# Performance work log

Measured on AMD Instinct MI355X. Metric: run time of the kernel, lower is better.

Reference implementation:

```python
import jax, jax.numpy as jnp
import numpy as np

B, N, DIM = 4, 2048, 1024
HEADS, DIM_HEAD = 16, 64
SCALE = DIM_HEAD ** -0.5


def setup_inputs() -> dict:
    key = jax.random.key(0)
    ks = jax.random.split(key, 5)
    x = jax.random.normal(ks[0], (B, N, DIM), dtype=jnp.float32)
    s = DIM ** -0.5
    Wq = jax.random.normal(ks[1], (DIM, HEADS * DIM_HEAD), dtype=jnp.float32) * s
    Wk = jax.random.normal(ks[2], (DIM, HEADS * DIM_HEAD), dtype=jnp.float32) * s
    Wv = jax.random.normal(ks[3], (DIM, HEADS * DIM_HEAD), dtype=jnp.float32) * s
    Wo = jax.random.normal(ks[4], (HEADS * DIM_HEAD, DIM), dtype=jnp.float32) * s
    bo = jnp.zeros((DIM,), dtype=jnp.float32)
    return {"x": x, "Wq": Wq, "Wk": Wk, "Wv": Wv, "Wo": Wo, "bo": bo}


def reference(x, Wq, Wk, Wv, Wo, bo):
    b, n, _ = x.shape
    # project and split heads: [b, n, h, d] -> [b, h, n, d]
    def split_heads(t):
        return t.reshape(b, n, HEADS, DIM_HEAD).transpose(0, 2, 1, 3)
    q = split_heads(x @ Wq)
    k = split_heads(x @ Wk)
    v = split_heads(x @ Wv)
    dots = jnp.einsum("bhid,bhjd->bhij", q, k) * SCALE  # [b,h,n,n]
    attn = jax.nn.softmax(dots, axis=-1)
    out = jnp.einsum("bhij,bhjd->bhid", attn, v)  # [b,h,n,d]
    out = out.transpose(0, 2, 1, 3).reshape(b, n, HEADS * DIM_HEAD)
    # project_out is True (heads != 1); dropout is identity at inference
    return out @ Wo + bo
```

## Files before the change

### kernel.cpp

```cpp
#include <hip/hip_runtime.h>
#include <stdint.h>

typedef __attribute__((ext_vector_type(8))) short short8;
typedef __attribute__((ext_vector_type(8))) unsigned short u16x8;
typedef __attribute__((ext_vector_type(4))) float f32x4;

#define DEV static __device__ __forceinline__

DEV unsigned short f2bf(float f) {
  unsigned u = __builtin_bit_cast(unsigned, f);
  u += 0x7FFF + ((u >> 16) & 1);
  return (unsigned short)(u >> 16);
}

DEV unsigned cvtpk_bf16(float lo, float hi) {
  unsigned r;
  asm("v_cvt_pk_bf16_f32 %0, %1, %2" : "=v"(r) : "v"(lo), "v"(hi));
  return r;
}

#define GLOAD16(gptr, lptr)                                                        \
  __builtin_amdgcn_global_load_lds((const __attribute__((address_space(1))) void*)(gptr), \
                                   (__attribute__((address_space(3))) void*)(lptr), 16, 0, 0)

__global__ __launch_bounds__(256) void k_cast_x(const float* __restrict__ in,
                                                unsigned short* __restrict__ out) {
  int idx = (blockIdx.x * 256 + threadIdx.x) * 8;
  float4 a = *(const float4*)(in + idx);
  float4 b = *(const float4*)(in + idx + 4);
  u16x8 v;
  v[0] = f2bf(a.x); v[1] = f2bf(a.y); v[2] = f2bf(a.z); v[3] = f2bf(a.w);
  v[4] = f2bf(b.x); v[5] = f2bf(b.y); v[6] = f2bf(b.z); v[7] = f2bf(b.w);
  *(u16x8*)(out + idx) = v;
}

__global__ __launch_bounds__(256) void k_transW(const float* __restrict__ wq,
                                                const float* __restrict__ wk,
                                                const float* __restrict__ wv,
                                                const float* __restrict__ wo,
                                                unsigned short* __restrict__ wqkvT,
                                                unsigned short* __restrict__ woT) {
  __shared__ __align__(16) unsigned short t[64 * 72];
  int z = blockIdx.z;
  const float* src = (z == 0) ? wq : (z == 1) ? wk : (z == 2) ? wv : wo;
  unsigned short* dst = (z < 3) ? (wqkvT + (size_t)z * 1048576) : woT;
  int r0 = blockIdx.y * 64;
  int c0 = blockIdx.x * 64;
  int tid = threadIdx.x;
#pragma unroll
  for (int it = 0; it < 4; ++it) {
    int idx = it * 256 + tid;
    int il = idx >> 4;
    int c4 = idx & 15;
    float4 v = *(const float4*)(src + (size_t)(r0 + il) * 1024 + c0 + c4 * 4);
    t[(c4 * 4 + 0) * 72 + il] = f2bf(v.x);
    t[(c4 * 4 + 1) * 72 + il] = f2bf(v.y);
    t[(c4 * 4 + 2) * 72 + il] = f2bf(v.z);
    t[(c4 * 4 + 3) * 72 + il] = f2bf(v.w);
  }
  __syncthreads();
#pragma unroll
  for (int it = 0; it < 2; ++it) {
    int idx = it * 256 + tid;
    int ol = idx >> 3;
    int ch = idx & 7;
    *(u16x8*)(dst + (size_t)(c0 + ol) * 1024 + r0 + ch * 8) =
        *(const u16x8*)(t + ol * 72 + ch * 8);
  }
}

template <int MODE>
__global__ __launch_bounds__(256) void k_gemm(const unsigned short* __restrict__ A,
                                              const unsigned short* __restrict__ Bt,
                                              unsigned short* __restrict__ outB,
                                              unsigned short* __restrict__ vTout,
                                              float* __restrict__ outF,
                                              const float* __restrict__ bias) {
  __shared__ __align__(16) unsigned short sA[128 * 64];
  __shared__ __align__(16) unsigned short sB[128 * 64];
  const int tid = threadIdx.x;
  const int l = tid & 63;
  const int w = tid >> 6;

  const int lid = blockIdx.x;
  const int nwg = (MODE == 0) ? 1536 : 512;
  const int swz = (lid & 7) * (nwg >> 3) + (lid >> 3);
  const int z = (MODE == 0) ? (swz >> 9) : 0;
  const int rem = (MODE == 0) ? (swz & 511) : swz;
  const int m0 = (rem >> 3) * 128;
  const int n0 = (rem & 7) * 128;

  const int wm = (w >> 1) * 64;
  const int wn = (w & 1) * 64;
  const int q16 = l & 15, g4 = l >> 4;
  const int lrow = l >> 3;
  const int lsw = ((l & 7) ^ lrow) * 8;

  const unsigned short* bt = Bt + (size_t)z * 1048576;
  unsigned short* dst = outB + (size_t)z * 8388608;
  const float sc = (MODE == 0 && z == 0) ? 0.125f * 1.44269504088896f : 1.0f;

  f32x4 acc[4][4];
#pragma unroll
  for (int i = 0; i < 4; ++i)
#pragma unroll
    for (int j = 0; j < 4; ++j) acc[i][j] = (f32x4){0.f, 0.f, 0.f, 0.f};

  for (int k0 = 0; k0 < 1024; k0 += 64) {
    __syncthreads();
#pragma unroll
    for (int r = 0; r < 4; ++r) {
      int chunk = w * 4 + r;
      int row = chunk * 8 + lrow;
      GLOAD16(A + (size_t)(m0 + row) * 1024 + k0 + lsw, sA + chunk * 512);
      GLOAD16(bt + (size_t)(n0 + row) * 1024 + k0 + lsw, sB + chunk * 512);
    }
    __syncthreads();
#pragma unroll
    for (int kk = 0; kk < 2; ++kk) {
      short8 af[4], bf_[4];
#pragma unroll
      for (int i = 0; i < 4; ++i) {
        int ra = wm + i * 16 + q16;
        af[i] = *(const short8*)(sA + ra * 64 + (((kk * 4 + g4) ^ (ra & 7)) * 8));
        int rb = wn + i * 16 + q16;
        bf_[i] = *(const short8*)(sB + rb * 64 + (((kk * 4 + g4) ^ (rb & 7)) * 8));
      }
#pragma unroll
      for (int mi = 0; mi < 4; ++mi)
#pragma unroll
        for (int ni = 0; ni < 4; ++ni)
          acc[mi][ni] =
              __builtin_amdgcn_mfma_f32_16x16x32_bf16(af[mi], bf_[ni], acc[mi][ni], 0, 0, 0);
    }
  }

  if (MODE == 0 && z == 2) {
#pragma unroll
    for (int mi = 0; mi < 4; ++mi) {
#pragma unroll
      for (int ni = 0; ni < 4; ++ni) {
        int row0 = m0 + wm + mi * 16 + g4 * 4;
        int col = n0 + wn + ni * 16 + q16;
        int b = row0 >> 11, seq0 = row0 & 2047;
        int h = col >> 6, d = col & 63;
        uint2 pv;
        pv.x = cvtpk_bf16(acc[mi][ni][0], acc[mi][ni][1]);
        pv.y = cvtpk_bf16(acc[mi][ni][2], acc[mi][ni][3]);
        *(uint2*)(vTout + (((size_t)(b * 16 + h) * 64 + d) * 2048 + seq0)) = pv;
      }
    }
  } else {
#pragma unroll
    for (int mi = 0; mi < 4; ++mi) {
#pragma unroll
      for (int ni = 0; ni < 4; ++ni) {
#pragma unroll
        for (int j = 0; j < 4; ++j) {
          int row = m0 + wm + mi * 16 + g4 * 4 + j;
          int col = n0 + wn + ni * 16 + q16;
          float val = acc[mi][ni][j];
          if (MODE == 0) {
            val *= sc;
            int b = row >> 11, seq = row & 2047;
            int h = col >> 6, d = col & 63;
            dst[((((size_t)b * 16 + h) * 2048 + seq) << 6) + d] = f2bf(val);
          } else {
            outF[(size_t)row * 1024 + col] = val + bias[col];
          }
        }
      }
    }
  }
}

__global__ __launch_bounds__(512) void k_attn(const unsigned short* __restrict__ Q,
                                              const unsigned short* __restrict__ Kg,
                                              const unsigned short* __restrict__ Vt,
                                              unsigned short* __restrict__ Oo) {
  __shared__ __align__(16) unsigned short sK[4][64 * 64];
  __shared__ __align__(16) unsigned short sV[4][64 * 64];
  __shared__ __align__(16) unsigned short sP[8][16 * 64];
  const int tid = threadIdx.x;
  const int l = tid & 63, w = tid >> 6;
  const int q16 = l & 15, g = l >> 4;
  const int bh = blockIdx.y;
  const int q0 = blockIdx.x * 128 + w * 16;
  const int lrow = l >> 3;
  const int lsw = ((l & 7) ^ lrow) * 8;

  const unsigned short* Qb = Q + ((size_t)bh * 2048 + q0) * 64;
  const unsigned short* Kb = Kg + (size_t)bh * 2048 * 64;
  const unsigned short* Vb = Vt + (size_t)bh * 64 * 2048;

  short8 qf[2];
#pragma unroll
  for (int s = 0; s < 2; ++s) qf[s] = *(const short8*)(Qb + q16 * 64 + s * 32 + g * 8);

  float sum = 0.f;
  f32x4 o[4];
#pragma unroll
  for (int dt = 0; dt < 4; ++dt) o[dt] = (f32x4){0.f, 0.f, 0.f, 0.f};

  auto STAGE = [&](int slot, int kv) {
    int row = w * 8 + lrow;
    GLOAD16(Kb + (size_t)(kv + row) * 64 + lsw, &sK[slot][w * 512]);
    GLOAD16(Vb + (size_t)row * 2048 + kv + lsw, &sV[slot][w * 512]);
  };

  auto COMPUTE = [&](int slot) {
    f32x4 st[4];
    __builtin_amdgcn_s_setprio(1);
#pragma unroll
    for (int t = 0; t < 4; ++t) {
      st[t] = (f32x4){0.f, 0.f, 0.f, 0.f};
#pragma unroll
      for (int s = 0; s < 2; ++s) {
        int key = t * 16 + q16;
        short8 kf = *(const short8*)(&sK[slot][key * 64 + (((s * 4 + g) ^ (key & 7)) * 8)]);
        st[t] = __builtin_amdgcn_mfma_f32_16x16x32_bf16(kf, qf[s], st[t], 0, 0, 0);
      }
    }
    __builtin_amdgcn_s_setprio(0);

    float p[4][4];
    float ps = 0.f;
#pragma unroll
    for (int t = 0; t < 4; ++t)
#pragma unroll
      for (int j = 0; j < 4; ++j) {
        p[t][j] = __builtin_amdgcn_exp2f(st[t][j]);
        ps += p[t][j];
      }
    ps += __shfl_xor(ps, 16);
    ps += __shfl_xor(ps, 32);
    sum += ps;

#pragma unroll
    for (int t = 0; t < 4; ++t) {
      uint2 pv;
      pv.x = cvtpk_bf16(p[t][0], p[t][1]);
      pv.y = cvtpk_bf16(p[t][2], p[t][3]);
      int c16 = t * 2 + (g >> 1);
      *(uint2*)(&sP[w][q16 * 64 + ((c16 ^ (q16 & 7)) * 8) + (g & 1) * 4]) = pv;
    }
    asm volatile("s_waitcnt lgkmcnt(0)" ::: "memory");
    __builtin_amdgcn_sched_barrier(0);

    __builtin_amdgcn_s_setprio(1);
#pragma unroll
    for (int win = 0; win < 2; ++win) {
      short8 pf = *(const short8*)(&sP[w][q16 * 64 + (((win * 4 + g) ^ (q16 & 7)) * 8)]);
#pragma unroll
      for (int dt = 0; dt < 4; ++dt) {
        int d = dt * 16 + q16;
        short8 vf = *(const short8*)(&sV[slot][d * 64 + (((win * 4 + g) ^ (d & 7)) * 8)]);
        o[dt] = __builtin_amdgcn_mfma_f32_16x16x32_bf16(pf, vf, o[dt], 0, 0, 0);
      }
    }
    __builtin_amdgcn_s_setprio(0);
  };

  STAGE(0, 0);
  STAGE(1, 64);
  asm volatile("s_waitcnt vmcnt(0)" ::: "memory");
  __syncthreads();

  for (int i = 0; i < 16; ++i) {
    const int sb = (i & 1) * 2;
    if (i < 15) {
      STAGE(sb ^ 2, (2 * i + 2) * 64);
      STAGE((sb ^ 2) + 1, (2 * i + 3) * 64);
    }
    COMPUTE(sb);
    COMPUTE(sb + 1);
    asm volatile("s_waitcnt vmcnt(0)" ::: "memory");
    __syncthreads();
  }

  float inv = 1.0f / sum;
  int b = bh >> 4, h = bh & 15;
#pragma unroll
  for (int j = 0; j < 4; ++j) {
    float ij = __shfl(inv, g * 4 + j);
#pragma unroll
    for (int dt = 0; dt < 4; ++dt)
      sP[w][(g * 4 + j) * 64 + dt * 16 + q16] = f2bf(o[dt][j] * ij);
  }
  unsigned short* Ob = Oo + ((size_t)b * 2048 + q0) * 1024 + h * 64;
#pragma unroll
  for (int it = 0; it < 2; ++it) {
    int flat = it * 512 + l * 8;
    int r = flat >> 6, c = flat & 63;
    *(u16x8*)(Ob + (size_t)r * 1024 + c) = *(const u16x8*)(&sP[w][r * 64 + c]);
  }
}

extern "C" void kernel_launch(void* const* d_in, const int* in_sizes, int n_in,
                              void* d_out, int out_size, void* d_ws, size_t ws_size,
                              hipStream_t stream) {
  const float* x = (const float*)d_in[0];
  const float* Wq = (const float*)d_in[1];
  const float* Wk = (const float*)d_in[2];
  const float* Wv = (const float*)d_in[3];
  const float* Wo = (const float*)d_in[4];
  const float* bo = (const float*)d_in[5];
  float* out = (float*)d_out;
  char* ws = (char*)d_ws;

  unsigned short* xb    = (unsigned short*)(ws);
  unsigned short* wqkvT = (unsigned short*)(ws + 16777216);
  unsigned short* woT   = (unsigned short*)(ws + 23068672);
  unsigned short* qkv   = (unsigned short*)(ws + 25165824);
  unsigned short* vT    = (unsigned short*)(ws + 75497472);
  unsigned short* aout  = xb;

  k_cast_x<<<4096, 256, 0, stream>>>(x, xb);
  k_transW<<<dim3(16, 16, 4), 256, 0, stream>>>(Wq, Wk, Wv, Wo, wqkvT, woT);
  k_gemm<0><<<1536, 256, 0, stream>>>(xb, wqkvT, qkv, vT, nullptr, nullptr);
  k_attn<<<dim3(16, 64), 512, 0, stream>>>(qkv, qkv + 8388608, vT, aout);
  k_gemm<1><<<512, 256, 0, stream>>>(aout, woT, nullptr, nullptr, out, bo);
}
```

Before: 201.8 us.

## Process two query tiles per wave in attention to reuse K/V fragments

Each wave now handles 32 query rows as two 16-row groups, so every K and V fragment read from LDS feeds two MFMAs. The block covers 256 queries, which halves the grid and the global K/V traffic per query. Blocks are remapped so that consecutive block IDs spread across heads. Staging moves from 4 slots with two tiles per barrier to a 2-slot double buffer with one tile per barrier, adding barriers and doubling accumulator registers. The launch bound of 4 blocks of 512 threads may limit registers.

```diff
diff --git a/kernel.cpp b/kernel.cpp
--- a/kernel.cpp
+++ b/kernel.cpp
@@ -174,75 +174,103 @@
   }
 }
 
-__global__ __launch_bounds__(512) void k_attn(const unsigned short* __restrict__ Q,
-                                              const unsigned short* __restrict__ Kg,
-                                              const unsigned short* __restrict__ Vt,
-                                              unsigned short* __restrict__ Oo) {
-  __shared__ __align__(16) unsigned short sK[4][64 * 64];
-  __shared__ __align__(16) unsigned short sV[4][64 * 64];
-  __shared__ __align__(16) unsigned short sP[8][16 * 64];
+__global__ __launch_bounds__(512, 4) void k_attn(const unsigned short* __restrict__ Q,
+                                                 const unsigned short* __restrict__ Kg,
+                                                 const unsigned short* __restrict__ Vt,
+                                                 unsigned short* __restrict__ Oo) {
+  __shared__ __align__(16) unsigned short sK[2][64 * 64];
+  __shared__ __align__(16) unsigned short sV[2][64 * 64];
+  __shared__ __align__(16) unsigned short sPa[8][16 * 64];
+  __shared__ __align__(16) unsigned short sPb[8][16 * 64];
   const int tid = threadIdx.x;
   const int l = tid & 63, w = tid >> 6;
   const int q16 = l & 15, g = l >> 4;
-  const int bh = blockIdx.y;
-  const int q0 = blockIdx.x * 128 + w * 16;
   const int lrow = l >> 3;
   const int lsw = ((l & 7) ^ lrow) * 8;
+
+  const int bid = blockIdx.x;
+  const int swz = (bid & 7) * 64 + (bid >> 3);
+  const int bh = swz >> 3;
+  const int q0 = (swz & 7) * 256 + w * 32;
 
   const unsigned short* Qb = Q + ((size_t)bh * 2048 + q0) * 64;
   const unsigned short* Kb = Kg + (size_t)bh * 2048 * 64;
   const unsigned short* Vb = Vt + (size_t)bh * 64 * 2048;
 
-  short8 qf[2];
-#pragma unroll
-  for (int s = 0; s < 2; ++s) qf[s] = *(const short8*)(Qb + q16 * 64 + s * 32 + g * 8);
-
-  float sum = 0.f;
-  f32x4 o[4];
-#pragma unroll
-  for (int dt = 0; dt < 4; ++dt) o[dt] = (f32x4){0.f, 0.f, 0.f, 0.f};
-
-  auto STAGE = [&](int slot, int kv) {
+  short8 qfa[2], qfb[2];
+#pragma unroll
+  for (int s = 0; s < 2; ++s) {
+    qfa[s] = *(const short8*)(Qb + q16 * 64 + s * 32 + g * 8);
+    qfb[s] = *(const short8*)(Qb + (16 + q16) * 64 + s * 32 + g * 8);
+  }
+
+  float suma = 0.f, sumb = 0.f;
+  f32x4 oa[4], ob[4];
+#pragma unroll
+  for (int dt = 0; dt < 4; ++dt) {
+    oa[dt] = (f32x4){0.f, 0.f, 0.f, 0.f};
+    ob[dt] = (f32x4){0.f, 0.f, 0.f, 0.f};
+  }
+
+  auto STAGE = [&](int buf, int kv) {
     int row = w * 8 + lrow;
-    GLOAD16(Kb + (size_t)(kv + row) * 64 + lsw, &sK[slot][w * 512]);
-    GLOAD16(Vb + (size_t)row * 2048 + kv + lsw, &sV[slot][w * 512]);
+    GLOAD16(Kb + (size_t)(kv + row) * 64 + lsw, &sK[buf][w * 512]);
+    GLOAD16(Vb + (size_t)row * 2048 + kv + lsw, &sV[buf][w * 512]);
   };
 
-  auto COMPUTE = [&](int slot) {
-    f32x4 st[4];
+  STAGE(0, 0);
+  asm volatile("s_waitcnt vmcnt(0)" ::: "memory");
+  __syncthreads();
+
+  for (int ti = 0; ti < 32; ++ti) {
+    const int cur = ti & 1;
+    if (ti < 31) STAGE(cur ^ 1, (ti + 1) * 64);
+
+    f32x4 sta[4], stb[4];
     __builtin_amdgcn_s_setprio(1);
 #pragma unroll
     for (int t = 0; t < 4; ++t) {
-      st[t] = (f32x4){0.f, 0.f, 0.f, 0.f};
+      sta[t] = (f32x4){0.f, 0.f, 0.f, 0.f};
+      stb[t] = (f32x4){0.f, 0.f, 0.f, 0.f};
 #pragma unroll
       for (int s = 0; s < 2; ++s) {
         int key = t * 16 + q16;
-        short8 kf = *(const short8*)(&sK[slot][key * 64 + (((s * 4 + g) ^ (key & 7)) * 8)]);
-        st[t] = __builtin_amdgcn_mfma_f32_16x16x32_bf16(kf, qf[s], st[t], 0, 0, 0);
+        short8 kf = *(const short8*)(&sK[cur][key * 64 + (((s * 4 + g) ^ (key & 7)) * 8)]);
+        sta[t] = __builtin_amdgcn_mfma_f32_16x16x32_bf16(kf, qfa[s], sta[t], 0, 0, 0);
+        stb[t] = __builtin_amdgcn_mfma_f32_16x16x32_bf16(kf, qfb[s], stb[t], 0, 0, 0);
       }
     }
     __builtin_amdgcn_s_setprio(0);
 
-    float p[4][4];
-    float ps = 0.f;
+    float pa[4][4], pb[4][4];
+    float psa = 0.f, psb = 0.f;
 #pragma unroll
     for (int t = 0; t < 4; ++t)
 #pragma unroll
       for (int j = 0; j < 4; ++j) {
-        p[t][j] = __builtin_amdgcn_exp2f(st[t][j]);
-        ps += p[t][j];
-      }
-    ps += __shfl_xor(ps, 16);
-    ps += __shfl_xor(ps, 32);
-    sum += ps;
+        pa[t][j] = __builtin_amdgcn_exp2f(sta[t][j]);
+        psa += pa[t][j];
+        pb[t][j] = __builtin_amdgcn_exp2f(stb[t][j]);
+        psb += pb[t][j];
+      }
+    psa += __shfl_xor(psa, 16);
+    psa += __shfl_xor(psa, 32);
+    psb += __shfl_xor(psb, 16);
+    psb += __shfl_xor(psb, 32);
+    suma += psa;
+    sumb += psb;
 
 #pragma unroll
     for (int t = 0; t < 4; ++t) {
+      int c16 = t * 2 + (g >> 1);
+      int off = q16 * 64 + ((c16 ^ (q16 & 7)) * 8) + (g & 1) * 4;
       uint2 pv;
-      pv.x = cvtpk_bf16(p[t][0], p[t][1]);
-      pv.y = cvtpk_bf16(p[t][2], p[t][3]);
-      int c16 = t * 2 + (g >> 1);
-      *(uint2*)(&sP[w][q16 * 64 + ((c16 ^ (q16 & 7)) * 8) + (g & 1) * 4]) = pv;
+      pv.x = cvtpk_bf16(pa[t][0], pa[t][1]);
+      pv.y = cvtpk_bf16(pa[t][2], pa[t][3]);
+      *(uint2*)(&sPa[w][off]) = pv;
+      pv.x = cvtpk_bf16(pb[t][0], pb[t][1]);
+      pv.y = cvtpk_bf16(pb[t][2], pb[t][3]);
+      *(uint2*)(&sPb[w][off]) = pv;
     }
     asm volatile("s_waitcnt lgkmcnt(0)" ::: "memory");
     __builtin_amdgcn_sched_barrier(0);
@@ -250,49 +278,42 @@
     __builtin_amdgcn_s_setprio(1);
 #pragma unroll
     for (int win = 0; win < 2; ++win) {
-      short8 pf = *(const short8*)(&sP[w][q16 * 64 + (((win * 4 + g) ^ (q16 & 7)) * 8)]);
+      int poff = q16 * 64 + (((win * 4 + g) ^ (q16 & 7)) * 8);
+      short8 pfa = *(const short8*)(&sPa[w][poff]);
+      short8 pfb = *(const short8*)(&sPb[w][poff]);
 #pragma unroll
       for (int dt = 0; dt < 4; ++dt) {
         int d = dt * 16 + q16;
-        short8 vf = *(const short8*)(&sV[slot][d * 64 + (((win * 4 + g) ^ (d & 7)) * 8)]);
-        o[dt] = __builtin_amdgcn_mfma_f32_16x16x32_bf16(pf, vf, o[dt], 0, 0, 0);
+        short8 vf = *(const short8*)(&sV[cur][d * 64 + (((win * 4 + g) ^ (d & 7)) * 8)]);
+        oa[dt] = __builtin_amdgcn_mfma_f32_16x16x32_bf16(pfa, vf, oa[dt], 0, 0, 0);
+        ob[dt] = __builtin_amdgcn_mfma_f32_16x16x32_bf16(pfb, vf, ob[dt], 0, 0, 0);
       }
     }
     __builtin_amdgcn_s_setprio(0);
-  };
-
-  STAGE(0, 0);
-  STAGE(1, 64);
-  asm volatile("s_waitcnt vmcnt(0)" ::: "memory");
-  __syncthreads();
-
-  for (int i = 0; i < 16; ++i) {
-    const int sb = (i & 1) * 2;
-    if (i < 15) {
-      STAGE(sb ^ 2, (2 * i + 2) * 64);
-      STAGE((sb ^ 2) + 1, (2 * i + 3) * 64);
-    }
-    COMPUTE(sb);
-    COMPUTE(sb + 1);
+
     asm volatile("s_waitcnt vmcnt(0)" ::: "memory");
     __syncthreads();
   }
 
-  float inv = 1.0f / sum;
+  float inva = 1.0f / suma, invb = 1.0f / sumb;
   int b = bh >> 4, h = bh & 15;
 #pragma unroll
   for (int j = 0; j < 4; ++j) {
-    float ij = __shfl(inv, g * 4 + j);
-#pragma unroll
-    for (int dt = 0; dt < 4; ++dt)
-      sP[w][(g * 4 + j) * 64 + dt * 16 + q16] = f2bf(o[dt][j] * ij);
+    float ija = __shfl(inva, g * 4 + j);
+    float ijb = __shfl(invb, g * 4 + j);
+#pragma unroll
+    for (int dt = 0; dt < 4; ++dt) {
+      sPa[w][(g * 4 + j) * 64 + dt * 16 + q16] = f2bf(oa[dt][j] * ija);
+      sPb[w][(g * 4 + j) * 64 + dt * 16 + q16] = f2bf(ob[dt][j] * ijb);
+    }
   }
   unsigned short* Ob = Oo + ((size_t)b * 2048 + q0) * 1024 + h * 64;
 #pragma unroll
-  for (int it = 0; it < 2; ++it) {
+  for (int it = 0; it < 4; ++it) {
     int flat = it * 512 + l * 8;
     int r = flat >> 6, c = flat & 63;
-    *(u16x8*)(Ob + (size_t)r * 1024 + c) = *(const u16x8*)(&sP[w][r * 64 + c]);
+    const unsigned short* src = (it < 2) ? &sPa[w][r * 64 + c] : &sPb[w][(r - 16) * 64 + c];
+    *(u16x8*)(Ob + (size_t)r * 1024 + c) = *(const u16x8*)src;
   }
 }
 
@@ -318,6 +339,6 @@
   k_cast_x<<<4096, 256, 0, stream>>>(x, xb);
   k_transW<<<dim3(16, 16, 4), 256, 0, stream>>>(Wq, Wk, Wv, Wo, wqkvT, woT);
   k_gemm<0><<<1536, 256, 0, stream>>>(xb, wqkvT, qkv, vT, nullptr, nullptr);
-  k_attn<<<dim3(16, 64), 512, 0, stream>>>(qkv, qkv + 8388608, vT, aout);
+  k_attn<<<512, 512, 0, stream>>>(qkv, qkv + 8388608, vT, aout);
   k_gemm<1><<<512, 256, 0, stream>>>(aout, woT, nullptr, nullptr, out, bo);
 }
```

Result: faster. 188.3 us, median of 3 (-6.7%).
